# Optimization experiments

Measured on AMD Instinct MI355X. Metric: run time of the kernel, lower is better.

The kernel has to match this reference:

```python
import jax, jax.numpy as jnp
import numpy as np

B, S, D, H = 4, 1024, 1024, 16
HS = D // H  # head_size = 64


def setup_inputs() -> dict:
    key = jax.random.key(0)
    ks = jax.random.split(key, 12)
    sc_d = 1.0 / np.sqrt(D)
    sc_h = 1.0 / np.sqrt(HS)
    inp = {
        "queries": jax.random.normal(ks[0], (B, S, D), jnp.float32),
        "keys": jax.random.normal(ks[1], (B, S, D), jnp.float32),
        "values": jax.random.normal(ks[2], (B, S, D), jnp.float32),
        # causal mask: scores where mask == 0 are filled with -1e9
        "mask": jnp.tril(jnp.ones((S, S), jnp.int32)),
        # per-head query/key projections: [H, D, HS] weights, [H, HS] biases
        "Wq": jax.random.uniform(ks[3], (H, D, HS), jnp.float32, -sc_d, sc_d),
        "bq": jax.random.uniform(ks[4], (H, HS), jnp.float32, -sc_d, sc_d),
        "Wk": jax.random.uniform(ks[5], (H, D, HS), jnp.float32, -sc_d, sc_d),
        "bk": jax.random.uniform(ks[6], (H, HS), jnp.float32, -sc_d, sc_d),
        # shared value projection: [D, HS]
        "Wv": jax.random.uniform(ks[7], (D, HS), jnp.float32, -sc_d, sc_d),
        "bv": jax.random.uniform(ks[8], (HS,), jnp.float32, -sc_d, sc_d),
        # output projection: [HS, D]
        "Wo": jax.random.uniform(ks[9], (HS, D), jnp.float32, -sc_h, sc_h),
        "bo": jax.random.uniform(ks[10], (D,), jnp.float32, -sc_h, sc_h),
    }
    return inp


def reference(queries, keys, values, mask, Wq, bq, Wk, bk, Wv, bv, Wo, bo):
    # shared value projection: [B, S, HS]
    v = jnp.einsum("bsd,de->bse", values, Wv) + bv
    # batched per-head projections (replaces the python loop over heads)
    q = jnp.einsum("bsd,hde->bhse", queries, Wq) + bq[None, :, None, :]
    k = jnp.einsum("btd,hde->bhte", keys, Wk) + bk[None, :, None, :]
    scores = jnp.einsum("bhse,bhte->bhst", q, k) / jnp.sqrt(jnp.float32(HS))
    scores = jnp.where(mask == 0, jnp.float32(-1e9), scores)
    attn = jax.nn.softmax(scores, axis=-1)  # [B, H, S, S]; dropout = eval-mode identity
    head_out = jnp.einsum("bhst,bte->bhse", attn, v)
    out = head_out.mean(axis=1)  # mean over heads -> [B, S, HS]
    out = jnp.einsum("bse,ed->bsd", out, Wo) + bo
    attention_weights = attn.mean(axis=1)  # [B, S, S]
    return out, attention_weights
```

## Files before the change

### kernel.cpp

```cpp
#include <hip/hip_runtime.h>
#include <hip/hip_bf16.h>
#include <stdint.h>

typedef _Float16 half8 __attribute__((ext_vector_type(8)));
typedef _Float16 half4 __attribute__((ext_vector_type(4)));
typedef float    f32x4 __attribute__((ext_vector_type(4)));

#define MFMA16(a, b, c) __builtin_amdgcn_mfma_f32_16x16x32_f16(a, b, c, 0, 0, 0)

typedef __attribute__((address_space(1))) const void GVOID;
typedef __attribute__((address_space(3))) void LVOID;
__device__ __forceinline__ void glds16(const void* g, void* l)
{
    __builtin_amdgcn_global_load_lds((GVOID*)g, (LVOID*)l, 16, 0, 0);
}

__global__ __launch_bounds__(256) void transpose_to_f16(
    const float* __restrict__ X, _Float16* __restrict__ Y,
    int R, int C, long inBS, long outBS)
{
    __shared__ float t[32][33];
    const int bz = blockIdx.z;
    X += (long)bz * inBS;
    Y += (long)bz * outBS;
    const int c0 = blockIdx.x * 32, r0 = blockIdx.y * 32;
    const int tx = threadIdx.x & 31, ty = threadIdx.x >> 5;
#pragma unroll
    for (int i = 0; i < 4; ++i)
        t[ty + i * 8][tx] = X[(long)(r0 + ty + i * 8) * C + c0 + tx];
    __syncthreads();
#pragma unroll
    for (int i = 0; i < 4; ++i)
        Y[(long)(c0 + ty + i * 8) * R + r0 + tx] = (_Float16)t[tx][ty + i * 8];
}

__global__ __launch_bounds__(256) void cvt_qk_f16(
    const float* __restrict__ S0, const float* __restrict__ S1,
    _Float16* __restrict__ D)
{
    const float* S = blockIdx.y ? S1 : S0;
    _Float16* Dz = D + (long)blockIdx.y * 4194304;
    const long i = ((long)blockIdx.x * 256 + threadIdx.x) * 8;
    const float4 v0 = *(const float4*)(S + i);
    const float4 v1 = *(const float4*)(S + i + 4);
    half8 h;
    h[0] = (_Float16)v0.x; h[1] = (_Float16)v0.y;
    h[2] = (_Float16)v0.z; h[3] = (_Float16)v0.w;
    h[4] = (_Float16)v1.x; h[5] = (_Float16)v1.y;
    h[6] = (_Float16)v1.z; h[7] = (_Float16)v1.w;
    *(half8*)(Dz + i) = h;
}

__global__ __launch_bounds__(256, 2) void gemm_qk_glds(
    const _Float16* __restrict__ A16,
    const _Float16* __restrict__ BT,
    const float* __restrict__ bias0, const float* __restrict__ bias1,
    _Float16* __restrict__ Cout)
{
    __shared__ __align__(16) _Float16 As[2][128 * 64];
    __shared__ __align__(16) _Float16 Bs[2][128 * 64];

    const int gx  = gridDim.x, gy = gridDim.y;
    const int nwg = gx * gy * (int)gridDim.z;
    const int lid = (int)blockIdx.x + gx * ((int)blockIdx.y + gy * (int)blockIdx.z);
    const int q8  = nwg >> 3;
    const int xcd = lid & 7, loc = lid >> 3;
    const int sw  = xcd * q8 + loc;
    const int nt  = sw % gx;
    const int tm2 = sw / gx;
    const int mt  = tm2 % gy;
    const int z   = tm2 / gy;

    const int n0 = nt * 128;
    const int m0 = mt * 128;
    const int tid  = threadIdx.x;
    const int wave = tid >> 6, lane = tid & 63;
    const int m16  = lane & 15, quad = lane >> 4;

    const char* Az = (const char*)(A16 + (long)z * 4194304);
    const char* Bz = (const char*)(BT  + (long)z * 1048576);

    const int colbyte = (((lane & 7) ^ (lane >> 3)) << 4);
    const char* gaBase = Az + ((long)(m0 + wave * 32 + (lane >> 3)) << 11) + colbyte;
    const char* gbBase = Bz + ((long)(n0 + wave * 32 + (lane >> 3)) << 11) + colbyte;

    f32x4 acc[2][8];
    {
        f32x4 zz = {0.f, 0.f, 0.f, 0.f};
#pragma unroll
        for (int i = 0; i < 2; ++i)
#pragma unroll
            for (int j = 0; j < 8; ++j) acc[i][j] = zz;
    }

    auto STAGE = [&](int bf, int k0) {
        const char* ga = gaBase + (k0 << 1);
        const char* gb = gbBase + (k0 << 1);
        _Float16* la = &As[bf][wave * 32 * 64];
        _Float16* lb = &Bs[bf][wave * 32 * 64];
#pragma unroll
        for (int i = 0; i < 4; ++i) {
            glds16(ga + (long)i * 8 * 2048, la + i * 8 * 64);
            glds16(gb + (long)i * 8 * 2048, lb + i * 8 * 64);
        }
    };

    auto COMPUTE = [&](int bf) {
        const char* Ab = (const char*)&As[bf][0];
        const char* Bp = (const char*)&Bs[bf][0];
        const int sw4 = (m16 & 7) << 4;
#pragma unroll
        for (int kss = 0; kss < 2; ++kss) {
            const int kbs = (kss * 64 + quad * 16) ^ sw4;
            const half8 a0 = *(const half8*)(Ab + (wave * 32 + m16) * 128 + kbs);
            const half8 a1 = *(const half8*)(Ab + (wave * 32 + 16 + m16) * 128 + kbs);
#pragma unroll
            for (int c = 0; c < 8; ++c) {
                const half8 bfr = *(const half8*)(Bp + (c * 16 + m16) * 128 + kbs);
                acc[0][c] = MFMA16(a0, bfr, acc[0][c]);
                acc[1][c] = MFMA16(a1, bfr, acc[1][c]);
            }
        }
    };

    STAGE(0, 0);
    __syncthreads();
    int cur = 0;
    for (int k0 = 0; k0 < 1024; k0 += 64) {
        if (k0 + 64 < 1024) STAGE(cur ^ 1, k0 + 64);
        COMPUTE(cur);
        __syncthreads();
        cur ^= 1;
    }

    const float* bias = z ? bias1 : bias0;
    _Float16* Cz = Cout + (long)z * 4194304;
#pragma unroll
    for (int hh = 0; hh < 2; ++hh) {
#pragma unroll
        for (int c = 0; c < 8; ++c) {
            const int col = n0 + c * 16 + m16;
            const float bb = bias[col];
#pragma unroll
            for (int r = 0; r < 4; ++r) {
                const int row = m0 + wave * 32 + hh * 16 + quad * 4 + r;
                Cz[(long)row * 1024 + col] = (_Float16)(acc[hh][c][r] + bb);
            }
        }
    }
}

__global__ __launch_bounds__(256, 2) void gemm_f16_v2(
    const float* __restrict__ A0, const float* __restrict__ A1,
    const _Float16* __restrict__ BT,
    const float* __restrict__ bias0, const float* __restrict__ bias1,
    void* __restrict__ Cout,
    int N, int lda, int ldbt, int ldc,
    long aBS, long bBS, long cBS,
    int c_half, int atomic, int nks, int kchunk)
{
    __shared__ __align__(16) _Float16 As[128][72];
    __shared__ __align__(16) _Float16 Bs[128][72];

    const int gx  = gridDim.x, gy = gridDim.y;
    const int nwg = gx * gy * (int)gridDim.z;
    const int lid = (int)blockIdx.x + gx * ((int)blockIdx.y + gy * (int)blockIdx.z);
    const int q8  = nwg >> 3, r8 = nwg & 7;
    const int xcd = lid & 7, loc = lid >> 3;
    const int sw  = (xcd < r8 ? xcd * (q8 + 1) : r8 * (q8 + 1) + (xcd - r8) * q8) + loc;
    const int nt  = sw % gx;
    const int tm2 = sw / gx;
    const int mt  = tm2 % gy;
    const int bz  = tm2 / gy;

    const int b = bz / nks, ks = bz % nks;
    const int kbeg = ks * kchunk;
    const int kend = kbeg + kchunk;

    const float* A = A1 ? (b ? A1 : A0) : (A0 + (long)b * aBS);
    const _Float16* Bb = BT + (long)b * bBS;

    const int n0 = nt * 128;
    const int m0 = mt * 128;
    const int tid  = threadIdx.x;
    const int wave = tid >> 6, lane = tid & 63;
    const int m16  = lane & 15, quad = lane >> 4;

    const int acol = (tid & 15) * 4;
    const int arb  = tid >> 4;
    const int bj   = tid >> 1;
    const int bcc  = (tid & 1) * 32;
    int jn = n0 + bj; if (jn > N - 1) jn = N - 1;
    const _Float16* bpB = Bb + (long)jn * ldbt;

    f32x4 acc[2][8];
    {
        f32x4 zz = {0.f, 0.f, 0.f, 0.f};
#pragma unroll
        for (int i = 0; i < 2; ++i)
#pragma unroll
            for (int j = 0; j < 8; ++j) acc[i][j] = zz;
    }

    for (int k0 = kbeg; k0 < kend; k0 += 64) {
        {
            const int cc = acol;
            float4 av[8];
#pragma unroll
            for (int p = 0; p < 8; ++p)
                av[p] = *(const float4*)(A + (long)(m0 + arb + p * 16) * lda + k0 + cc);
#pragma unroll
            for (int p = 0; p < 8; ++p) {
                half4 hv;
                hv[0] = (_Float16)av[p].x; hv[1] = (_Float16)av[p].y;
                hv[2] = (_Float16)av[p].z; hv[3] = (_Float16)av[p].w;
                *(half4*)&As[arb + p * 16][cc] = hv;
            }
        }
        {
            const _Float16* bp = bpB + k0 + bcc;
            half8 b0 = *(const half8*)(bp);
            half8 b1 = *(const half8*)(bp + 8);
            half8 b2 = *(const half8*)(bp + 16);
            half8 b3 = *(const half8*)(bp + 24);
            *(half8*)&Bs[bj][bcc]      = b0;
            *(half8*)&Bs[bj][bcc + 8]  = b1;
            *(half8*)&Bs[bj][bcc + 16] = b2;
            *(half8*)&Bs[bj][bcc + 24] = b3;
        }
        __syncthreads();
#pragma unroll
        for (int kss = 0; kss < 2; ++kss) {
            const int ko = kss * 32 + quad * 8;
            const half8 a0 = *(const half8*)&As[wave * 32 + m16][ko];
            const half8 a1 = *(const half8*)&As[wave * 32 + 16 + m16][ko];
#pragma unroll
            for (int c = 0; c < 8; ++c) {
                const half8 bf = *(const half8*)&Bs[c * 16 + m16][ko];
                acc[0][c] = MFMA16(a0, bf, acc[0][c]);
                acc[1][c] = MFMA16(a1, bf, acc[1][c]);
            }
        }
        __syncthreads();
    }

    const float* bias = b ? bias1 : bias0;
    const int addb = (bias != nullptr) && (kbeg == 0);
#pragma unroll
    for (int hh = 0; hh < 2; ++hh) {
#pragma unroll
        for (int c = 0; c < 8; ++c) {
            const int col = n0 + c * 16 + m16;
            if (col >= N) continue;
            const float bb = addb ? bias[col] : 0.f;
#pragma unroll
            for (int r = 0; r < 4; ++r) {
                const int row = m0 + wave * 32 + hh * 16 + quad * 4 + r;
                const float v = acc[hh][c][r] + bb;
                const long idx = (long)b * cBS + (long)row * ldc + col;
                if (atomic)      atomicAdd(&((float*)Cout)[idx], v);
                else if (c_half) ((_Float16*)Cout)[idx] = (_Float16)v;
                else             ((float*)Cout)[idx] = v;
            }
        }
    }
}

__global__ __launch_bounds__(256, 2) void attn_stats(
    const _Float16* __restrict__ q_all, const _Float16* __restrict__ k_all,
    float* __restrict__ m_out, float* __restrict__ il_out)
{
    const int st = blockIdx.x, h = blockIdx.y, b = blockIdx.z;
    const int tid = threadIdx.x, wave = tid >> 6, lane = tid & 63;
    const int m16 = lane & 15, quad = lane >> 4;
    const int s0 = st * 64;
    const int sw = s0 + wave * 16;

    __shared__ __align__(16) _Float16 qs[64][72];
    __shared__ __align__(16) _Float16 ks[64][72];

    const int srow = tid >> 2;
    const int scol = (tid & 3) * 16;

    {
        const _Float16* qsrc = q_all + ((long)(b * 1024 + s0 + srow)) * 1024 + h * 64 + scol;
        *(half8*)&qs[srow][scol]     = *(const half8*)(qsrc);
        *(half8*)&qs[srow][scol + 8] = *(const half8*)(qsrc + 8);
    }

    const _Float16* ksrcb = k_all + ((long)(b * 1024 + srow)) * 1024 + h * 64 + scol;

    float mr[4], lr[4];
#pragma unroll
    for (int r = 0; r < 4; ++r) { mr[r] = -3.0e38f; lr[r] = 0.f; }

    half8 a0, a1;
    for (int tt = 0; tt <= st; ++tt) {
        const _Float16* ksrc = ksrcb + (long)(tt * 64) * 1024;
        const half8 k0 = *(const half8*)(ksrc);
        const half8 k1 = *(const half8*)(ksrc + 8);

        __syncthreads();
        *(half8*)&ks[srow][scol]     = k0;
        *(half8*)&ks[srow][scol + 8] = k1;
        __syncthreads();

        if (tt == 0) {
            a0 = *(const half8*)&qs[wave * 16 + m16][quad * 8];
            a1 = *(const half8*)&qs[wave * 16 + m16][quad * 8 + 32];
        }

        if (tt < st) {
#pragma unroll
            for (int c = 0; c < 4; ++c) {
                const half8 b0 = *(const half8*)&ks[c * 16 + m16][quad * 8];
                const half8 b1 = *(const half8*)&ks[c * 16 + m16][quad * 8 + 32];
                f32x4 cc = {0.f, 0.f, 0.f, 0.f};
                cc = MFMA16(a0, b0, cc);
                cc = MFMA16(a1, b1, cc);
#pragma unroll
                for (int r = 0; r < 4; ++r) {
                    const float zz = cc[r] * 0.125f;
                    const float nm = fmaxf(mr[r], zz);
                    lr[r] = lr[r] * __expf(mr[r] - nm) + __expf(zz - nm);
                    mr[r] = nm;
                }
            }
        } else {
#pragma unroll
            for (int c = 0; c < 4; ++c) {
                const half8 b0 = *(const half8*)&ks[c * 16 + m16][quad * 8];
                const half8 b1 = *(const half8*)&ks[c * 16 + m16][quad * 8 + 32];
                f32x4 cc = {0.f, 0.f, 0.f, 0.f};
                cc = MFMA16(a0, b0, cc);
                cc = MFMA16(a1, b1, cc);
                const int col = tt * 64 + c * 16 + m16;
#pragma unroll
                for (int r = 0; r < 4; ++r) {
                    const int row = sw + quad * 4 + r;
                    if (col <= row) {
                        const float zz = cc[r] * 0.125f;
                        const float nm = fmaxf(mr[r], zz);
                        lr[r] = lr[r] * __expf(mr[r] - nm) + __expf(zz - nm);
                        mr[r] = nm;
                    }
                }
            }
        }
    }

#pragma unroll
    for (int mk = 1; mk < 16; mk <<= 1) {
#pragma unroll
        for (int r = 0; r < 4; ++r) {
            const float om = __shfl_xor(mr[r], mk);
            const float ol = __shfl_xor(lr[r], mk);
            const float nm = fmaxf(mr[r], om);
            lr[r] = lr[r] * __expf(mr[r] - nm) + ol * __expf(om - nm);
            mr[r] = nm;
        }
    }
    if (m16 == 0) {
#pragma unroll
        for (int r = 0; r < 4; ++r) {
            const long idx = ((long)(b * 16 + h)) * 1024 + sw + quad * 4 + r;
            m_out[idx]  = mr[r];
            il_out[idx] = 1.f / lr[r];
        }
    }
}

__global__ __launch_bounds__(256, 2) void attn_pmean(
    const _Float16* __restrict__ q_all, const _Float16* __restrict__ k_all,
    const float* __restrict__ m_in, const float* __restrict__ il_in,
    float* __restrict__ attn)
{
    const int ttile = blockIdx.x, stile = blockIdx.y, b = blockIdx.z;
    const int tid = threadIdx.x;
    if (ttile > stile) {
        const int c4 = (tid & 15) * 4;
        float4 zz = {0.f, 0.f, 0.f, 0.f};
#pragma unroll
        for (int i = 0; i < 4; ++i) {
            const int r = stile * 64 + (tid >> 4) + i * 16;
            *(float4*)&attn[((long)(b * 1024 + r)) * 1024 + ttile * 64 + c4] = zz;
        }
        return;
    }

    __shared__ __align__(16) _Float16 qs[64][72];
    __shared__ __align__(16) _Float16 ks[64][72];

    const int wave = tid >> 6, lane = tid & 63;
    const int m16 = lane & 15, quad = lane >> 4;
    const int s0 = stile * 64;
    const int t0 = ttile * 64;
    const int sw = s0 + wave * 16;
    const int diag = (ttile == stile);

    const int srow = tid >> 2;
    const int scol = (tid & 3) * 16;

    const _Float16* qsrc = q_all + ((long)(b * 1024 + s0 + srow)) * 1024 + scol;
    const _Float16* ksrc = k_all + ((long)(b * 1024 + t0 + srow)) * 1024 + scol;
    const long sbase = ((long)(b * 16)) * 1024 + sw + quad * 4;

    float pm[4][4];
#pragma unroll
    for (int c = 0; c < 4; ++c)
#pragma unroll
        for (int r = 0; r < 4; ++r) pm[c][r] = 0.f;

    for (int h = 0; h < 16; ++h) {
        const int ho = h * 64;
        const half8 q0 = *(const half8*)(qsrc + ho);
        const half8 q1 = *(const half8*)(qsrc + ho + 8);
        const half8 k0 = *(const half8*)(ksrc + ho);
        const half8 k1 = *(const half8*)(ksrc + ho + 8);
        const long idx = sbase + (long)h * 1024;
        const float4 mv = *(const float4*)&m_in[idx];
        const float4 iv = *(const float4*)&il_in[idx];

        __syncthreads();
        *(half8*)&qs[srow][scol]     = q0;
        *(half8*)&qs[srow][scol + 8] = q1;
        *(half8*)&ks[srow][scol]     = k0;
        *(half8*)&ks[srow][scol + 8] = k1;
        __syncthreads();

        const half8 a0 = *(const half8*)&qs[wave * 16 + m16][quad * 8];
        const half8 a1 = *(const half8*)&qs[wave * 16 + m16][quad * 8 + 32];
        const float mrow[4] = {mv.x, mv.y, mv.z, mv.w};
        const float irow[4] = {iv.x, iv.y, iv.z, iv.w};

        if (!diag) {
#pragma unroll
            for (int c = 0; c < 4; ++c) {
                const half8 b0 = *(const half8*)&ks[c * 16 + m16][quad * 8];
                const half8 b1 = *(const half8*)&ks[c * 16 + m16][quad * 8 + 32];
                f32x4 cc = {0.f, 0.f, 0.f, 0.f};
                cc = MFMA16(a0, b0, cc);
                cc = MFMA16(a1, b1, cc);
#pragma unroll
                for (int r = 0; r < 4; ++r)
                    pm[c][r] += __expf(cc[r] * 0.125f - mrow[r]) * irow[r];
            }
        } else {
#pragma unroll
            for (int c = 0; c < 4; ++c) {
                const half8 b0 = *(const half8*)&ks[c * 16 + m16][quad * 8];
                const half8 b1 = *(const half8*)&ks[c * 16 + m16][quad * 8 + 32];
                f32x4 cc = {0.f, 0.f, 0.f, 0.f};
                cc = MFMA16(a0, b0, cc);
                cc = MFMA16(a1, b1, cc);
                const int col = t0 + c * 16 + m16;
#pragma unroll
                for (int r = 0; r < 4; ++r) {
                    const int row = sw + quad * 4 + r;
                    if (col <= row)
                        pm[c][r] += __expf(cc[r] * 0.125f - mrow[r]) * irow[r];
                }
            }
        }
    }

#pragma unroll
    for (int c = 0; c < 4; ++c) {
#pragma unroll
        for (int r = 0; r < 4; ++r) {
            const int row = sw + quad * 4 + r;
            const int col = t0 + c * 16 + m16;
            attn[((long)(b * 1024 + row)) * 1024 + col] = pm[c][r] * 0.0625f;
        }
    }
}

extern "C" void kernel_launch(void* const* d_in, const int* in_sizes, int n_in,
                              void* d_out, int out_size, void* d_ws, size_t ws_size,
                              hipStream_t stream)
{
    const float* queries = (const float*)d_in[0];
    const float* keys    = (const float*)d_in[1];
    const float* values  = (const float*)d_in[2];
    const float* Wq = (const float*)d_in[4];
    const float* bq = (const float*)d_in[5];
    const float* Wk = (const float*)d_in[6];
    const float* bk = (const float*)d_in[7];
    const float* Wv = (const float*)d_in[8];
    const float* bv = (const float*)d_in[9];
    const float* Wo = (const float*)d_in[10];
    const float* bo = (const float*)d_in[11];

    float* out_ptr  = (float*)d_out;
    float* attn_ptr = out_ptr + (long)4096 * 1024;

    uint8_t* w = (uint8_t*)d_ws;
    size_t off = 0;
    auto alloc = [&](size_t bytes) {
        void* p = w + off;
        off = (off + bytes + 255) & ~(size_t)255;
        return p;
    };
    _Float16* WqkT  = (_Float16*)alloc((size_t)2 * 1024 * 1024 * 2);
    _Float16* WvT   = (_Float16*)alloc((size_t)64 * 1024 * 2);
    _Float16* WoT   = (_Float16*)alloc((size_t)1024 * 64 * 2);
    _Float16* qkall = (_Float16*)alloc((size_t)2 * 4194304 * 2);
    _Float16* a16   = (_Float16*)alloc((size_t)2 * 4194304 * 2);
    float*    vbuf  = (float*)alloc((size_t)4096 * 64 * 4);
    _Float16* vT    = (_Float16*)alloc((size_t)4 * 64 * 1024 * 2);
    float*    ctx   = (float*)alloc((size_t)4096 * 64 * 4);
    float*    mbuf  = (float*)alloc((size_t)65536 * 4);
    float*    ilbuf = (float*)alloc((size_t)65536 * 4);
    (void)ws_size; (void)in_sizes; (void)n_in; (void)out_size;

    _Float16* qall = qkall;
    _Float16* kall = qkall + (long)4194304;

    transpose_to_f16<<<dim3(2, 32, 16), 256, 0, stream>>>(Wq, WqkT, 1024, 64, 65536, 65536);
    transpose_to_f16<<<dim3(2, 32, 16), 256, 0, stream>>>(Wk, WqkT + (long)1024 * 1024, 1024, 64, 65536, 65536);
    transpose_to_f16<<<dim3(2, 32, 1),  256, 0, stream>>>(Wv, WvT, 1024, 64, 0, 0);
    transpose_to_f16<<<dim3(32, 2, 1),  256, 0, stream>>>(Wo, WoT, 64, 1024, 0, 0);
    cvt_qk_f16<<<dim3(2048, 2, 1), 256, 0, stream>>>(queries, keys, a16);

    gemm_qk_glds<<<dim3(8, 32, 2), 256, 0, stream>>>(
        a16, WqkT, bq, bk, qkall);

    hipMemsetAsync(vbuf, 0, (size_t)4096 * 64 * 4, stream);
    gemm_f16_v2<<<dim3(1, 32, 8), 256, 0, stream>>>(
        values, nullptr, WvT, bv, nullptr, vbuf,
        64, 1024, 1024, 64,
        0, 0, 0,
        0, 1, 8, 128);

    transpose_to_f16<<<dim3(2, 32, 4), 256, 0, stream>>>(vbuf, vT, 1024, 64, 65536, 65536);

    attn_stats<<<dim3(16, 16, 4), 256, 0, stream>>>(qall, kall, mbuf, ilbuf);
    attn_pmean<<<dim3(16, 16, 4), 256, 0, stream>>>(qall, kall, mbuf, ilbuf, attn_ptr);

    hipMemsetAsync(ctx, 0, (size_t)4096 * 64 * 4, stream);
    gemm_f16_v2<<<dim3(1, 8, 32), 256, 0, stream>>>(
        attn_ptr, nullptr, vT, nullptr, nullptr, ctx,
        64, 1024, 1024, 64,
        (long)1048576, (long)65536, (long)65536,
        0, 1, 8, 128);

    gemm_f16_v2<<<dim3(8, 32, 1), 256, 0, stream>>>(
        ctx, nullptr, WoT, bo, nullptr, out_ptr,
        1024, 64, 64, 1024,
        0, 0, 0,
        0, 0, 1, 64);
}
```

Baseline: 252.9 us.

## Fuse head-mean attention times V into pmean kernel with atomic ctx accumulation

```diff
diff --git a/kernel.cpp b/kernel.cpp
--- a/kernel.cpp
+++ b/kernel.cpp
@@ -266,7 +266,7 @@
     }
 }
 
-__global__ __launch_bounds__(256, 2) void attn_stats(
+__global__ __launch_bounds__(256, 4) void attn_stats(
     const _Float16* __restrict__ q_all, const _Float16* __restrict__ k_all,
     float* __restrict__ m_out, float* __restrict__ il_out)
 {
@@ -370,10 +370,12 @@
     }
 }
 
-__global__ __launch_bounds__(256, 2) void attn_pmean(
+__global__ __launch_bounds__(256, 4) void attn_pmean(
     const _Float16* __restrict__ q_all, const _Float16* __restrict__ k_all,
     const float* __restrict__ m_in, const float* __restrict__ il_in,
-    float* __restrict__ attn)
+    const _Float16* __restrict__ vT,
+    float* __restrict__ attn,
+    float* __restrict__ ctx)
 {
     const int ttile = blockIdx.x, stile = blockIdx.y, b = blockIdx.z;
     const int tid = threadIdx.x;
@@ -390,6 +392,7 @@
 
     __shared__ __align__(16) _Float16 qs[64][72];
     __shared__ __align__(16) _Float16 ks[64][72];
+    __shared__ __align__(16) _Float16 ps[64][72];
 
     const int wave = tid >> 6, lane = tid & 63;
     const int m16 = lane & 15, quad = lane >> 4;
@@ -468,9 +471,38 @@
     for (int c = 0; c < 4; ++c) {
 #pragma unroll
         for (int r = 0; r < 4; ++r) {
+            const int rloc = (wave << 4) + (quad << 2) + r;
+            const int cloc = c * 16 + m16;
+            const float p = pm[c][r] * 0.0625f;
+            attn[((long)(b * 1024 + s0 + rloc)) * 1024 + t0 + cloc] = p;
+            ps[rloc][cloc] = (_Float16)p;
+        }
+    }
+    __syncthreads();
+
+    const _Float16* vTb = vT + (long)b * 65536 + t0;
+    f32x4 apv[4];
+    {
+        f32x4 zz = {0.f, 0.f, 0.f, 0.f};
+#pragma unroll
+        for (int c = 0; c < 4; ++c) apv[c] = zz;
+    }
+#pragma unroll
+    for (int kss = 0; kss < 2; ++kss) {
+        const half8 a = *(const half8*)&ps[wave * 16 + m16][kss * 32 + quad * 8];
+#pragma unroll
+        for (int c = 0; c < 4; ++c) {
+            const half8 bf = *(const half8*)(vTb + (long)(c * 16 + m16) * 1024 + kss * 32 + quad * 8);
+            apv[c] = MFMA16(a, bf, apv[c]);
+        }
+    }
+#pragma unroll
+    for (int c = 0; c < 4; ++c) {
+#pragma unroll
+        for (int r = 0; r < 4; ++r) {
             const int row = sw + quad * 4 + r;
-            const int col = t0 + c * 16 + m16;
-            attn[((long)(b * 1024 + row)) * 1024 + col] = pm[c][r] * 0.0625f;
+            const int e   = c * 16 + m16;
+            atomicAdd(&ctx[((long)(b * 1024 + row)) * 64 + e], apv[c][r]);
         }
     }
 }
@@ -534,15 +566,9 @@
 
     transpose_to_f16<<<dim3(2, 32, 4), 256, 0, stream>>>(vbuf, vT, 1024, 64, 65536, 65536);
 
+    hipMemsetAsync(ctx, 0, (size_t)4096 * 64 * 4, stream);
     attn_stats<<<dim3(16, 16, 4), 256, 0, stream>>>(qall, kall, mbuf, ilbuf);
-    attn_pmean<<<dim3(16, 16, 4), 256, 0, stream>>>(qall, kall, mbuf, ilbuf, attn_ptr);
-
-    hipMemsetAsync(ctx, 0, (size_t)4096 * 64 * 4, stream);
-    gemm_f16_v2<<<dim3(1, 8, 32), 256, 0, stream>>>(
-        attn_ptr, nullptr, vT, nullptr, nullptr, ctx,
-        64, 1024, 1024, 64,
-        (long)1048576, (long)65536, (long)65536,
-        0, 1, 8, 128);
+    attn_pmean<<<dim3(16, 16, 4), 256, 0, stream>>>(qall, kall, mbuf, ilbuf, vT, attn_ptr, ctx);
 
     gemm_f16_v2<<<dim3(8, 32, 1), 256, 0, stream>>>(
         ctx, nullptr, WoT, bo, nullptr, out_ptr,
```

After: 241.8 us. -4.4%, faster.
